# Kernel optimization log

Hardware: AMD Instinct MI355X
Metric: run time of the kernel (lower is better)

The kernel has to match this reference:

```python
import jax, jax.numpy as jnp
import numpy as np

N_NODES = 100000
N_EDGES = 2000000
D = 128
HIDDEN = 128


def setup_inputs() -> dict:
    key = jax.random.key(0)
    k_src, k_dst, k_idx, k_w1, k_w2 = jax.random.split(key, 5)
    src = jax.random.normal(k_src, (N_NODES, D), dtype=jnp.float32)
    dst = jax.random.normal(k_dst, (N_NODES, D), dtype=jnp.float32)
    edge_label_index = jax.random.randint(k_idx, (2, N_EDGES), 0, N_NODES, dtype=jnp.int64)
    # Kaiming-ish init for the two linear layers
    W1 = jax.random.normal(k_w1, (D, HIDDEN), dtype=jnp.float32) / np.sqrt(D)
    b1 = jnp.zeros((HIDDEN,), dtype=jnp.float32)
    W2 = jax.random.normal(k_w2, (HIDDEN, 1), dtype=jnp.float32) / np.sqrt(HIDDEN)
    b2 = jnp.zeros((1,), dtype=jnp.float32)
    return {"src": src, "dst": dst, "edge_label_index": edge_label_index,
            "W1": W1, "b1": b1, "W2": W2, "b2": b2}


def reference(src, dst, edge_label_index, W1, b1, W2, b2):
    row = edge_label_index[0]
    col = edge_label_index[1]
    # gather endpoint embeddings and fuse with elementwise product: [E, D]
    z = src[row] * dst[col]
    # 2-layer MLP; dropout p=0 is the identity
    h = jax.nn.relu(z @ W1 + b1)           # [E, HIDDEN]
    out = h @ W2 + b2                       # [E, 1]
    return out.reshape(-1)                  # [E]
```

## Files before the change

### kernel.cpp

```cpp
#include <hip/hip_runtime.h>
#include <hip/hip_bf16.h>

typedef __attribute__((ext_vector_type(8))) short short8;
typedef __attribute__((ext_vector_type(4))) float f32x4;

#define BLOCK 256
#define GTILE 16

__device__ __forceinline__ int swz16(int row, int boff) {
    return (row << 8) + (boff ^ ((row & 15) << 4));
}
__device__ __forceinline__ int swzH(int row, int boff) {
    return (row << 7) + (boff ^ ((row & 7) << 4));
}

__global__ __launch_bounds__(256) void cvt_bf16_kernel(
    const float* __restrict__ a, const float* __restrict__ b,
    __hip_bfloat16* __restrict__ oa, __hip_bfloat16* __restrict__ ob, int n)
{
    const int i = blockIdx.x * blockDim.x + threadIdx.x;
    const int stride = gridDim.x * blockDim.x;
    const float4* a4 = (const float4*)a;
    const float4* b4 = (const float4*)b;
    const int n8 = n >> 3;
    for (int j = i; j < n8; j += stride) {
        float4 x0 = a4[2 * j], x1 = a4[2 * j + 1];
        float4 y0 = b4[2 * j], y1 = b4[2 * j + 1];
        union { __hip_bfloat16 h[8]; uint4 u; } pa, pb;
        pa.h[0]=__float2bfloat16(x0.x); pa.h[1]=__float2bfloat16(x0.y);
        pa.h[2]=__float2bfloat16(x0.z); pa.h[3]=__float2bfloat16(x0.w);
        pa.h[4]=__float2bfloat16(x1.x); pa.h[5]=__float2bfloat16(x1.y);
        pa.h[6]=__float2bfloat16(x1.z); pa.h[7]=__float2bfloat16(x1.w);
        pb.h[0]=__float2bfloat16(y0.x); pb.h[1]=__float2bfloat16(y0.y);
        pb.h[2]=__float2bfloat16(y0.z); pb.h[3]=__float2bfloat16(y0.w);
        pb.h[4]=__float2bfloat16(y1.x); pb.h[5]=__float2bfloat16(y1.y);
        pb.h[6]=__float2bfloat16(y1.z); pb.h[7]=__float2bfloat16(y1.w);
        ((uint4*)oa)[j] = pa.u;
        ((uint4*)ob)[j] = pb.u;
    }
    for (int j = (n8 << 3) + i; j < n; j += stride) {
        oa[j] = __float2bfloat16(a[j]);
        ob[j] = __float2bfloat16(b[j]);
    }
}

template<bool BF16G>
__global__ __launch_bounds__(BLOCK, 3) void edge_mlp_kernel(
    const float* __restrict__ srcf, const float* __restrict__ dstf,
    const __hip_bfloat16* __restrict__ srcb, const __hip_bfloat16* __restrict__ dstb,
    const int*   __restrict__ eli,
    const float* __restrict__ W1, const float* __restrict__ b1,
    const float* __restrict__ W2, const float* __restrict__ b2,
    float* __restrict__ out, int E)
{
    __shared__ __align__(16) char lds[49152];

    const int tid  = threadIdx.x;
    const int lane = tid & 63;
    const int w    = tid >> 6;
    const int rr   = lane & 15;
    const int kgrp = lane >> 4;
    const int rq8  = lane >> 3;
    const int cl   = lane & 7;

    for (int idx = tid; idx < 128 * 128; idx += BLOCK) {
        int k = idx >> 7, n = idx & 127;
        *(__hip_bfloat16*)(lds + swz16(n, k * 2)) = __float2bfloat16(W1[idx]);
    }
    int probe = eli[2 * (lane & 31) + 1];
    unsigned long long bl = __ballot(lane < 32 && probe != 0);
    const int i64f = (bl == 0ull) ? 1 : 0;
    __syncthreads();

    char* zb = lds + 32768 + (w << 12);

    float b1s[8], w2s[8];
    #pragma unroll
    for (int cb = 0; cb < 8; ++cb) {
        b1s[cb] = b1[cb * 16 + rr];
        w2s[cb] = W2[cb * 16 + rr];
    }
    const float bias2 = b2[0];

    const int ngroups = (E + GTILE - 1) / GTILE;
    const int step = gridDim.x * 4;
    int g = blockIdx.x * 4 + w;
    if (g >= ngroups) return;

    auto idxload = [&](int gg) -> int {
        gg = gg < ngroups ? gg : ngroups - 1;
        int e = gg * GTILE + rr; if (e >= E) e = E - 1;
        size_t off = (lane < 32) ? (size_t)e : (size_t)E + (size_t)e;
        return i64f ? eli[2 * off] : eli[off];
    };

    auto loadT = [&](int iv, short8 (&s)[4], short8 (&d)[4]) {
        const short8* s8 = (const short8*)srcb;
        const short8* d8 = (const short8*)dstb;
        #pragma unroll
        for (int i = 0; i < 4; ++i) {
            int hr = i * 8 + rq8;
            int e  = hr >> 1, h = hr & 1;
            int r = __shfl(iv, e, 64);
            int c = __shfl(iv, 32 + e, 64);
            s[i] = s8[(size_t)r * 16 + h * 8 + cl];
            d[i] = d8[(size_t)c * 16 + h * 8 + cl];
        }
    };
    auto writeT = [&](const short8 (&s)[4], const short8 (&d)[4]) {
        #pragma unroll
        for (int i = 0; i < 4; ++i) {
            int hr = i * 8 + rq8;
            union { __hip_bfloat16 h[8]; short8 v; } pr;
            #pragma unroll
            for (int j = 0; j < 8; ++j) {
                float fs = __bfloat162float(((const __hip_bfloat16*)&s[i])[j]);
                float fd = __bfloat162float(((const __hip_bfloat16*)&d[i])[j]);
                pr.h[j] = __float2bfloat16(fs * fd);
            }
            *(short8*)(zb + swzH(hr, cl * 16)) = pr.v;
        }
    };
    auto stageF = [&](int iv) {
        const float4* s4 = (const float4*)srcf;
        const float4* d4 = (const float4*)dstf;
        #pragma unroll
        for (int i = 0; i < 4; ++i) {
            int hr = i * 8 + rq8;
            int e  = hr >> 1, h = hr & 1;
            int r = __shfl(iv, e, 64);
            int c = __shfl(iv, 32 + e, 64);
            float4 a0 = s4[(size_t)r * 32 + h * 16 + cl * 2];
            float4 a1 = s4[(size_t)r * 32 + h * 16 + cl * 2 + 1];
            float4 c0 = d4[(size_t)c * 32 + h * 16 + cl * 2];
            float4 c1 = d4[(size_t)c * 32 + h * 16 + cl * 2 + 1];
            union { __hip_bfloat16 hh[8]; short8 v; } pr;
            pr.hh[0] = __float2bfloat16(a0.x * c0.x);
            pr.hh[1] = __float2bfloat16(a0.y * c0.y);
            pr.hh[2] = __float2bfloat16(a0.z * c0.z);
            pr.hh[3] = __float2bfloat16(a0.w * c0.w);
            pr.hh[4] = __float2bfloat16(a1.x * c1.x);
            pr.hh[5] = __float2bfloat16(a1.y * c1.y);
            pr.hh[6] = __float2bfloat16(a1.z * c1.z);
            pr.hh[7] = __float2bfloat16(a1.w * c1.w);
            *(short8*)(zb + swzH(hr, cl * 16)) = pr.v;
        }
    };

    auto compute = [&](int gg) {
        f32x4 acc[8];
        #pragma unroll
        for (int cb = 0; cb < 8; ++cb) acc[cb] = (f32x4){0.f, 0.f, 0.f, 0.f};
        __builtin_amdgcn_s_setprio(1);
        #pragma unroll
        for (int kk = 0; kk < 4; ++kk) {
            short8 af = *(const short8*)(zb + swzH(rr * 2 + (kk >> 1),
                                                   (kk & 1) * 64 + kgrp * 16));
            #pragma unroll
            for (int cb = 0; cb < 8; ++cb) {
                short8 bf = *(const short8*)(lds + swz16(cb * 16 + rr,
                                                         kk * 64 + kgrp * 16));
                acc[cb] = __builtin_amdgcn_mfma_f32_16x16x32_bf16(af, bf, acc[cb], 0, 0, 0);
            }
        }
        __builtin_amdgcn_s_setprio(0);
        #pragma unroll
        for (int r = 0; r < 4; ++r) {
            float p = 0.f;
            #pragma unroll
            for (int cb = 0; cb < 8; ++cb) {
                float h = acc[cb][r] + b1s[cb];
                h = fmaxf(h, 0.f);
                p = fmaf(h, w2s[cb], p);
            }
            p += __shfl_xor(p, 1, 64);
            p += __shfl_xor(p, 2, 64);
            p += __shfl_xor(p, 4, 64);
            p += __shfl_xor(p, 8, 64);
            int e = gg * GTILE + kgrp * 4 + r;
            if (rr == 0 && e < E)
                __builtin_nontemporal_store(p + bias2, &out[e]);
        }
    };

    if constexpr (BF16G) {
        short8 svA[4], dvA[4], svB[4], dvB[4];
        int iv0 = idxload(g);
        int iv1 = idxload(g + step);
        loadT(iv0, svA, dvA);
        loadT(iv1, svB, dvB);
        int iv2 = idxload(g + 2 * step);

        while (true) {
            asm volatile("" ::: "memory");
            writeT(svA, dvA);
            loadT(iv2, svA, dvA);
            iv2 = idxload(g + 3 * step);
            asm volatile("" ::: "memory");
            compute(g);
            g += step; if (g >= ngroups) break;

            asm volatile("" ::: "memory");
            writeT(svB, dvB);
            loadT(iv2, svB, dvB);
            iv2 = idxload(g + 3 * step);
            asm volatile("" ::: "memory");
            compute(g);
            g += step; if (g >= ngroups) break;
        }
    } else {
        for (; g < ngroups; g += step) {
            asm volatile("" ::: "memory");
            int iv = idxload(g);
            stageF(iv);
            asm volatile("" ::: "memory");
            compute(g);
        }
    }
}

extern "C" void kernel_launch(void* const* d_in, const int* in_sizes, int n_in,
                              void* d_out, int out_size, void* d_ws, size_t ws_size,
                              hipStream_t stream) {
    const float* src = (const float*)d_in[0];
    const float* dst = (const float*)d_in[1];
    const int*   eli = (const int*)d_in[2];
    const float* W1  = (const float*)d_in[3];
    const float* b1  = (const float*)d_in[4];
    const float* W2  = (const float*)d_in[5];
    const float* b2  = (const float*)d_in[6];
    float* out = (float*)d_out;

    const int E = in_sizes[2] / 2;
    const int nsrc = in_sizes[0];
    const size_t need = (size_t)(in_sizes[0] + in_sizes[1]) * sizeof(__hip_bfloat16);
    const int ngroups = (E + GTILE - 1) / GTILE;
    int nblocks = (ngroups + 3) / 4;
    int grid = nblocks < 768 ? nblocks : 768;

    if (ws_size >= need) {
        __hip_bfloat16* srcb = (__hip_bfloat16*)d_ws;
        __hip_bfloat16* dstb = srcb + nsrc;
        cvt_bf16_kernel<<<dim3(2048), dim3(256), 0, stream>>>(src, dst, srcb, dstb, nsrc);
        edge_mlp_kernel<true><<<dim3(grid), dim3(BLOCK), 0, stream>>>(
            src, dst, srcb, dstb, eli, W1, b1, W2, b2, out, E);
    } else {
        edge_mlp_kernel<false><<<dim3(grid), dim3(BLOCK), 0, stream>>>(
            src, dst, (const __hip_bfloat16*)nullptr, (const __hip_bfloat16*)nullptr,
            eli, W1, b1, W2, b2, out, E);
    }
}
```

Baseline: 178.0 us.

## Bucket edges by destination node and process buckets per XCD for locality

Adds a histogram, scan and scatter pass that sorts edges into 32 buckets by destination node index. The MLP kernel then processes each bucket on a fixed subset of blocks (blockIdx mod 8), so the dst rows being gathered stay resident in a local cache. A final permute kernel writes the results back in the original edge order. It also switches the gathered tables from bf16 to fp16 and does the elementwise product with packed half multiplies. In exchange it adds several extra kernel launches and global passes over the 2M-edge index array, plus a memset.

```diff
diff --git a/kernel.cpp b/kernel.cpp
--- a/kernel.cpp
+++ b/kernel.cpp
@@ -1,11 +1,13 @@
 #include <hip/hip_runtime.h>
 #include <hip/hip_bf16.h>
-
-typedef __attribute__((ext_vector_type(8))) short short8;
+#include <hip/hip_fp16.h>
+
+typedef __attribute__((ext_vector_type(8))) _Float16 half8;
 typedef __attribute__((ext_vector_type(4))) float f32x4;
 
 #define BLOCK 256
 #define GTILE 16
+#define NBKT  32
 
 __device__ __forceinline__ int swz16(int row, int boff) {
     return (row << 8) + (boff ^ ((row & 15) << 4));
@@ -14,10 +16,24 @@
     return (row << 7) + (boff ^ ((row & 7) << 4));
 }
 
-__global__ __launch_bounds__(256) void cvt_bf16_kernel(
+__device__ __forceinline__ int probe_i64(const int* eli) {
+    int any = 0;
+    #pragma unroll
+    for (int i = 0; i < 32; ++i) any |= eli[2 * i + 1];
+    return (any == 0) ? 1 : 0;
+}
+
+__global__ __launch_bounds__(256) void cvt_hist_kernel(
     const float* __restrict__ a, const float* __restrict__ b,
-    __hip_bfloat16* __restrict__ oa, __hip_bfloat16* __restrict__ ob, int n)
-{
+    _Float16* __restrict__ oa, _Float16* __restrict__ ob, int n,
+    const int* __restrict__ eli, int E, float scale, unsigned int* __restrict__ cnt)
+{
+    __shared__ unsigned int h[NBKT];
+    __shared__ int s_i64;
+    if (threadIdx.x < NBKT) h[threadIdx.x] = 0;
+    if (threadIdx.x == 0) s_i64 = probe_i64(eli);
+    __syncthreads();
+
     const int i = blockIdx.x * blockDim.x + threadIdx.x;
     const int stride = gridDim.x * blockDim.x;
     const float4* a4 = (const float4*)a;
@@ -26,32 +42,92 @@
     for (int j = i; j < n8; j += stride) {
         float4 x0 = a4[2 * j], x1 = a4[2 * j + 1];
         float4 y0 = b4[2 * j], y1 = b4[2 * j + 1];
-        union { __hip_bfloat16 h[8]; uint4 u; } pa, pb;
-        pa.h[0]=__float2bfloat16(x0.x); pa.h[1]=__float2bfloat16(x0.y);
-        pa.h[2]=__float2bfloat16(x0.z); pa.h[3]=__float2bfloat16(x0.w);
-        pa.h[4]=__float2bfloat16(x1.x); pa.h[5]=__float2bfloat16(x1.y);
-        pa.h[6]=__float2bfloat16(x1.z); pa.h[7]=__float2bfloat16(x1.w);
-        pb.h[0]=__float2bfloat16(y0.x); pb.h[1]=__float2bfloat16(y0.y);
-        pb.h[2]=__float2bfloat16(y0.z); pb.h[3]=__float2bfloat16(y0.w);
-        pb.h[4]=__float2bfloat16(y1.x); pb.h[5]=__float2bfloat16(y1.y);
-        pb.h[6]=__float2bfloat16(y1.z); pb.h[7]=__float2bfloat16(y1.w);
+        union { _Float16 hh[8]; uint4 u; } pa, pb;
+        pa.hh[0]=(_Float16)x0.x; pa.hh[1]=(_Float16)x0.y;
+        pa.hh[2]=(_Float16)x0.z; pa.hh[3]=(_Float16)x0.w;
+        pa.hh[4]=(_Float16)x1.x; pa.hh[5]=(_Float16)x1.y;
+        pa.hh[6]=(_Float16)x1.z; pa.hh[7]=(_Float16)x1.w;
+        pb.hh[0]=(_Float16)y0.x; pb.hh[1]=(_Float16)y0.y;
+        pb.hh[2]=(_Float16)y0.z; pb.hh[3]=(_Float16)y0.w;
+        pb.hh[4]=(_Float16)y1.x; pb.hh[5]=(_Float16)y1.y;
+        pb.hh[6]=(_Float16)y1.z; pb.hh[7]=(_Float16)y1.w;
         ((uint4*)oa)[j] = pa.u;
         ((uint4*)ob)[j] = pb.u;
     }
     for (int j = (n8 << 3) + i; j < n; j += stride) {
-        oa[j] = __float2bfloat16(a[j]);
-        ob[j] = __float2bfloat16(b[j]);
-    }
-}
-
-template<bool BF16G>
-__global__ __launch_bounds__(BLOCK, 3) void edge_mlp_kernel(
-    const float* __restrict__ srcf, const float* __restrict__ dstf,
-    const __hip_bfloat16* __restrict__ srcb, const __hip_bfloat16* __restrict__ dstb,
-    const int*   __restrict__ eli,
+        oa[j] = (_Float16)a[j];
+        ob[j] = (_Float16)b[j];
+    }
+    const int i64f = s_i64;
+    for (int e = i; e < E; e += stride) {
+        int c = i64f ? eli[2 * ((size_t)E + e)] : eli[(size_t)E + e];
+        int bkt = (int)((float)c * scale);
+        if (bkt > NBKT - 1) bkt = NBKT - 1;
+        atomicAdd(&h[bkt], 1u);
+    }
+    __syncthreads();
+    if (threadIdx.x < NBKT && h[threadIdx.x])
+        atomicAdd(&cnt[threadIdx.x], h[threadIdx.x]);
+}
+
+__global__ void scan_kernel(const unsigned int* __restrict__ cnt,
+                            unsigned int* __restrict__ segStart,
+                            unsigned int* __restrict__ cursor)
+{
+    if (threadIdx.x == 0) {
+        unsigned int s = 0;
+        for (int b = 0; b < NBKT; ++b) { segStart[b] = s; cursor[b] = s; s += cnt[b]; }
+        segStart[NBKT] = s;
+    }
+}
+
+__global__ __launch_bounds__(256) void scatter_kernel(
+    const int* __restrict__ eli, int E, float scale,
+    unsigned int* __restrict__ cursor,
+    uint2* __restrict__ sorted, unsigned int* __restrict__ inv)
+{
+    __shared__ unsigned int lcnt[NBKT];
+    __shared__ unsigned int lpos[NBKT];
+    __shared__ int s_i64;
+    if (threadIdx.x < NBKT) lcnt[threadIdx.x] = 0;
+    if (threadIdx.x == 0) s_i64 = probe_i64(eli);
+    __syncthreads();
+    const int i64f = s_i64;
+
+    const int chunk = (E + gridDim.x - 1) / gridDim.x;
+    const int e0 = blockIdx.x * chunk;
+    const int e1 = min(E, e0 + chunk);
+
+    for (int e = e0 + threadIdx.x; e < e1; e += blockDim.x) {
+        int c = i64f ? eli[2 * ((size_t)E + e)] : eli[(size_t)E + e];
+        int bkt = (int)((float)c * scale);
+        if (bkt > NBKT - 1) bkt = NBKT - 1;
+        atomicAdd(&lcnt[bkt], 1u);
+    }
+    __syncthreads();
+    if (threadIdx.x < NBKT) {
+        unsigned int nv = lcnt[threadIdx.x];
+        lpos[threadIdx.x] = nv ? atomicAdd(&cursor[threadIdx.x], nv) : 0u;
+    }
+    __syncthreads();
+    for (int e = e0 + threadIdx.x; e < e1; e += blockDim.x) {
+        int r, c;
+        if (i64f) { r = eli[2 * (size_t)e]; c = eli[2 * ((size_t)E + e)]; }
+        else      { r = eli[e];             c = eli[(size_t)E + e]; }
+        int bkt = (int)((float)c * scale);
+        if (bkt > NBKT - 1) bkt = NBKT - 1;
+        unsigned int pos = atomicAdd(&lpos[bkt], 1u);
+        sorted[pos] = make_uint2((unsigned)r, (unsigned)c);
+        inv[e] = pos;
+    }
+}
+
+__global__ __launch_bounds__(BLOCK, 3) void mlp_sorted_kernel(
+    const _Float16* __restrict__ srcb, const _Float16* __restrict__ dstb,
+    const uint2* __restrict__ sorted, const unsigned int* __restrict__ segStart,
     const float* __restrict__ W1, const float* __restrict__ b1,
     const float* __restrict__ W2, const float* __restrict__ b2,
-    float* __restrict__ out, int E)
+    float* __restrict__ tmp, int E)
 {
     __shared__ __align__(16) char lds[49152];
 
@@ -65,7 +141,149 @@
 
     for (int idx = tid; idx < 128 * 128; idx += BLOCK) {
         int k = idx >> 7, n = idx & 127;
-        *(__hip_bfloat16*)(lds + swz16(n, k * 2)) = __float2bfloat16(W1[idx]);
+        *(_Float16*)(lds + swz16(n, k * 2)) = (_Float16)W1[idx];
+    }
+    __syncthreads();
+
+    char* zb = lds + 32768 + (w << 12);
+
+    float b1s[8], w2s[8];
+    #pragma unroll
+    for (int cb = 0; cb < 8; ++cb) {
+        b1s[cb] = b1[cb * 16 + rr];
+        w2s[cb] = W2[cb * 16 + rr];
+    }
+    const float bias2 = b2[0];
+
+    const int x     = blockIdx.x & 7;
+    const int kb    = blockIdx.x >> 3;
+    const int nbs   = gridDim.x >> 3;
+    const int wslot = kb * 4 + w;
+    const int wstep = nbs * 4;
+
+    half8 sv[4], dv[4];
+    const half8* s8 = (const half8*)srcb;
+    const half8* d8 = (const half8*)dstb;
+
+    for (int j = 0; j < NBKT / 8; ++j) {
+        const int b  = x + 8 * j;
+        const int s0 = (int)segStart[b];
+        const int s1 = (int)segStart[b + 1];
+        if (s1 <= s0) continue;
+        const int nt = (s1 - s0 + 15) >> 4;
+        int t = wslot;
+        if (t >= nt) continue;
+
+        {
+            int idx = s0 + t * 16 + rr; if (idx >= s1) idx = s1 - 1;
+            uint2 iv = sorted[idx];
+            #pragma unroll
+            for (int i = 0; i < 4; ++i) {
+                int hr = i * 8 + rq8, e = hr >> 1, hh = hr & 1;
+                int r = __shfl((int)iv.x, e, 64);
+                int c = __shfl((int)iv.y, e, 64);
+                sv[i] = s8[(size_t)r * 16 + hh * 8 + cl];
+                dv[i] = d8[(size_t)c * 16 + hh * 8 + cl];
+            }
+        }
+
+        while (true) {
+            const int base = s0 + t * 16;
+            int cnt = s1 - base; if (cnt > 16) cnt = 16;
+
+            asm volatile("" ::: "memory");
+            #pragma unroll
+            for (int i = 0; i < 4; ++i) {
+                int hr = i * 8 + rq8;
+                half8 pr = sv[i] * dv[i];
+                *(half8*)(zb + swzH(hr, cl * 16)) = pr;
+            }
+
+            const int tn = t + wstep;
+            if (tn < nt) {
+                int idx = s0 + tn * 16 + rr; if (idx >= s1) idx = s1 - 1;
+                uint2 iv = sorted[idx];
+                #pragma unroll
+                for (int i = 0; i < 4; ++i) {
+                    int hr = i * 8 + rq8, e = hr >> 1, hh = hr & 1;
+                    int r = __shfl((int)iv.x, e, 64);
+                    int c = __shfl((int)iv.y, e, 64);
+                    sv[i] = s8[(size_t)r * 16 + hh * 8 + cl];
+                    dv[i] = d8[(size_t)c * 16 + hh * 8 + cl];
+                }
+            }
+            asm volatile("" ::: "memory");
+
+            f32x4 acc[8];
+            #pragma unroll
+            for (int cb = 0; cb < 8; ++cb) acc[cb] = (f32x4){0.f, 0.f, 0.f, 0.f};
+            __builtin_amdgcn_s_setprio(1);
+            #pragma unroll
+            for (int kk = 0; kk < 4; ++kk) {
+                half8 af = *(const half8*)(zb + swzH(rr * 2 + (kk >> 1),
+                                                     (kk & 1) * 64 + kgrp * 16));
+                #pragma unroll
+                for (int cb = 0; cb < 8; ++cb) {
+                    half8 bf = *(const half8*)(lds + swz16(cb * 16 + rr,
+                                                           kk * 64 + kgrp * 16));
+                    acc[cb] = __builtin_amdgcn_mfma_f32_16x16x32_f16(af, bf, acc[cb], 0, 0, 0);
+                }
+            }
+            __builtin_amdgcn_s_setprio(0);
+
+            #pragma unroll
+            for (int r = 0; r < 4; ++r) {
+                float p = 0.f;
+                #pragma unroll
+                for (int cb = 0; cb < 8; ++cb) {
+                    float hv = acc[cb][r] + b1s[cb];
+                    hv = fmaxf(hv, 0.f);
+                    p = fmaf(hv, w2s[cb], p);
+                }
+                p += __shfl_xor(p, 1, 64);
+                p += __shfl_xor(p, 2, 64);
+                p += __shfl_xor(p, 4, 64);
+                p += __shfl_xor(p, 8, 64);
+                int eo = kgrp * 4 + r;
+                if (rr == 0 && eo < cnt)
+                    __builtin_nontemporal_store(p + bias2, &tmp[base + eo]);
+            }
+            if (tn >= nt) break;
+            t = tn;
+        }
+    }
+}
+
+__global__ __launch_bounds__(256) void permute_kernel(
+    const float* __restrict__ tmp, const unsigned int* __restrict__ inv,
+    float* __restrict__ out, int E)
+{
+    for (int e = blockIdx.x * blockDim.x + threadIdx.x; e < E;
+         e += gridDim.x * blockDim.x)
+        out[e] = tmp[inv[e]];
+}
+
+template<int MODE>
+__global__ __launch_bounds__(BLOCK, 3) void edge_mlp_fb(
+    const float* __restrict__ srcf, const float* __restrict__ dstf,
+    const _Float16* __restrict__ srcb, const _Float16* __restrict__ dstb,
+    const int* __restrict__ eli,
+    const float* __restrict__ W1, const float* __restrict__ b1,
+    const float* __restrict__ W2, const float* __restrict__ b2,
+    float* __restrict__ out, int E)
+{
+    __shared__ __align__(16) char lds[49152];
+    const int tid  = threadIdx.x;
+    const int lane = tid & 63;
+    const int w    = tid >> 6;
+    const int rr   = lane & 15;
+    const int kgrp = lane >> 4;
+    const int rq8  = lane >> 3;
+    const int cl   = lane & 7;
+
+    for (int idx = tid; idx < 128 * 128; idx += BLOCK) {
+        int k = idx >> 7, n = idx & 127;
+        *(_Float16*)(lds + swz16(n, k * 2)) = (_Float16)W1[idx];
     }
     int probe = eli[2 * (lane & 31) + 1];
     unsigned long long bl = __ballot(lane < 32 && probe != 0);
@@ -73,7 +291,6 @@
     __syncthreads();
 
     char* zb = lds + 32768 + (w << 12);
-
     float b1s[8], w2s[8];
     #pragma unroll
     for (int cb = 0; cb < 8; ++cb) {
@@ -94,31 +311,17 @@
         return i64f ? eli[2 * off] : eli[off];
     };
 
-    auto loadT = [&](int iv, short8 (&s)[4], short8 (&d)[4]) {
-        const short8* s8 = (const short8*)srcb;
-        const short8* d8 = (const short8*)dstb;
+    half8 sv[4], dv[4];
+    auto loadT = [&](int iv) {
+        const half8* s8 = (const half8*)srcb;
+        const half8* d8 = (const half8*)dstb;
         #pragma unroll
         for (int i = 0; i < 4; ++i) {
-            int hr = i * 8 + rq8;
-            int e  = hr >> 1, h = hr & 1;
+            int hr = i * 8 + rq8, e = hr >> 1, hh = hr & 1;
             int r = __shfl(iv, e, 64);
             int c = __shfl(iv, 32 + e, 64);
-            s[i] = s8[(size_t)r * 16 + h * 8 + cl];
-            d[i] = d8[(size_t)c * 16 + h * 8 + cl];
-        }
-    };
-    auto writeT = [&](const short8 (&s)[4], const short8 (&d)[4]) {
-        #pragma unroll
-        for (int i = 0; i < 4; ++i) {
-            int hr = i * 8 + rq8;
-            union { __hip_bfloat16 h[8]; short8 v; } pr;
-            #pragma unroll
-            for (int j = 0; j < 8; ++j) {
-                float fs = __bfloat162float(((const __hip_bfloat16*)&s[i])[j]);
-                float fd = __bfloat162float(((const __hip_bfloat16*)&d[i])[j]);
-                pr.h[j] = __float2bfloat16(fs * fd);
-            }
-            *(short8*)(zb + swzH(hr, cl * 16)) = pr.v;
+            sv[i] = s8[(size_t)r * 16 + hh * 8 + cl];
+            dv[i] = d8[(size_t)c * 16 + hh * 8 + cl];
         }
     };
     auto stageF = [&](int iv) {
@@ -126,27 +329,21 @@
         const float4* d4 = (const float4*)dstf;
         #pragma unroll
         for (int i = 0; i < 4; ++i) {
-            int hr = i * 8 + rq8;
-            int e  = hr >> 1, h = hr & 1;
+            int hr = i * 8 + rq8, e = hr >> 1, hh = hr & 1;
             int r = __shfl(iv, e, 64);
             int c = __shfl(iv, 32 + e, 64);
-            float4 a0 = s4[(size_t)r * 32 + h * 16 + cl * 2];
-            float4 a1 = s4[(size_t)r * 32 + h * 16 + cl * 2 + 1];
-            float4 c0 = d4[(size_t)c * 32 + h * 16 + cl * 2];
-            float4 c1 = d4[(size_t)c * 32 + h * 16 + cl * 2 + 1];
-            union { __hip_bfloat16 hh[8]; short8 v; } pr;
-            pr.hh[0] = __float2bfloat16(a0.x * c0.x);
-            pr.hh[1] = __float2bfloat16(a0.y * c0.y);
-            pr.hh[2] = __float2bfloat16(a0.z * c0.z);
-            pr.hh[3] = __float2bfloat16(a0.w * c0.w);
-            pr.hh[4] = __float2bfloat16(a1.x * c1.x);
-            pr.hh[5] = __float2bfloat16(a1.y * c1.y);
-            pr.hh[6] = __float2bfloat16(a1.z * c1.z);
-            pr.hh[7] = __float2bfloat16(a1.w * c1.w);
-            *(short8*)(zb + swzH(hr, cl * 16)) = pr.v;
+            float4 a0 = s4[(size_t)r * 32 + hh * 16 + cl * 2];
+            float4 a1 = s4[(size_t)r * 32 + hh * 16 + cl * 2 + 1];
+            float4 c0 = d4[(size_t)c * 32 + hh * 16 + cl * 2];
+            float4 c1 = d4[(size_t)c * 32 + hh * 16 + cl * 2 + 1];
+            union { _Float16 hf[8]; half8 v; } pr;
+            pr.hf[0]=(_Float16)(a0.x*c0.x); pr.hf[1]=(_Float16)(a0.y*c0.y);
+            pr.hf[2]=(_Float16)(a0.z*c0.z); pr.hf[3]=(_Float16)(a0.w*c0.w);
+            pr.hf[4]=(_Float16)(a1.x*c1.x); pr.hf[5]=(_Float16)(a1.y*c1.y);
+            pr.hf[6]=(_Float16)(a1.z*c1.z); pr.hf[7]=(_Float16)(a1.w*c1.w);
+            *(half8*)(zb + swzH(hr, cl * 16)) = pr.v;
         }
     };
-
     auto compute = [&](int gg) {
         f32x4 acc[8];
         #pragma unroll
@@ -154,13 +351,13 @@
         __builtin_amdgcn_s_setprio(1);
         #pragma unroll
         for (int kk = 0; kk < 4; ++kk) {
-            short8 af = *(const short8*)(zb + swzH(rr * 2 + (kk >> 1),
-                                                   (kk & 1) * 64 + kgrp * 16));
+            half8 af = *(const half8*)(zb + swzH(rr * 2 + (kk >> 1),
+                                                 (kk & 1) * 64 + kgrp * 16));
             #pragma unroll
             for (int cb = 0; cb < 8; ++cb) {
-                short8 bf = *(const short8*)(lds + swz16(cb * 16 + rr,
-                                                         kk * 64 + kgrp * 16));
-                acc[cb] = __builtin_amdgcn_mfma_f32_16x16x32_bf16(af, bf, acc[cb], 0, 0, 0);
+                half8 bf = *(const half8*)(lds + swz16(cb * 16 + rr,
+                                                       kk * 64 + kgrp * 16));
+                acc[cb] = __builtin_amdgcn_mfma_f32_16x16x32_f16(af, bf, acc[cb], 0, 0, 0);
             }
         }
         __builtin_amdgcn_s_setprio(0);
@@ -169,9 +366,9 @@
             float p = 0.f;
             #pragma unroll
             for (int cb = 0; cb < 8; ++cb) {
-                float h = acc[cb][r] + b1s[cb];
-                h = fmaxf(h, 0.f);
-                p = fmaf(h, w2s[cb], p);
+                float hv = acc[cb][r] + b1s[cb];
+                hv = fmaxf(hv, 0.f);
+                p = fmaf(hv, w2s[cb], p);
             }
             p += __shfl_xor(p, 1, 64);
             p += __shfl_xor(p, 2, 64);
@@ -183,30 +380,23 @@
         }
     };
 
-    if constexpr (BF16G) {
-        short8 svA[4], dvA[4], svB[4], dvB[4];
-        int iv0 = idxload(g);
-        int iv1 = idxload(g + step);
-        loadT(iv0, svA, dvA);
-        loadT(iv1, svB, dvB);
-        int iv2 = idxload(g + 2 * step);
-
+    if constexpr (MODE == 1) {
+        int iv = idxload(g);
+        loadT(iv);
         while (true) {
             asm volatile("" ::: "memory");
-            writeT(svA, dvA);
-            loadT(iv2, svA, dvA);
-            iv2 = idxload(g + 3 * step);
+            #pragma unroll
+            for (int i = 0; i < 4; ++i) {
+                int hr = i * 8 + rq8;
+                half8 pr = sv[i] * dv[i];
+                *(half8*)(zb + swzH(hr, cl * 16)) = pr;
+            }
+            int gn = g + step;
+            if (gn < ngroups) { int iv2 = idxload(gn); loadT(iv2); }
             asm volatile("" ::: "memory");
             compute(g);
-            g += step; if (g >= ngroups) break;
-
-            asm volatile("" ::: "memory");
-            writeT(svB, dvB);
-            loadT(iv2, svB, dvB);
-            iv2 = idxload(g + 3 * step);
-            asm volatile("" ::: "memory");
-            compute(g);
-            g += step; if (g >= ngroups) break;
+            if (gn >= ngroups) break;
+            g = gn;
         }
     } else {
         for (; g < ngroups; g += step) {
@@ -232,21 +422,64 @@
     float* out = (float*)d_out;
 
     const int E = in_sizes[2] / 2;
-    const int nsrc = in_sizes[0];
-    const size_t need = (size_t)(in_sizes[0] + in_sizes[1]) * sizeof(__hip_bfloat16);
-    const int ngroups = (E + GTILE - 1) / GTILE;
-    int nblocks = (ngroups + 3) / 4;
-    int grid = nblocks < 768 ? nblocks : 768;
-
-    if (ws_size >= need) {
-        __hip_bfloat16* srcb = (__hip_bfloat16*)d_ws;
-        __hip_bfloat16* dstb = srcb + nsrc;
-        cvt_bf16_kernel<<<dim3(2048), dim3(256), 0, stream>>>(src, dst, srcb, dstb, nsrc);
-        edge_mlp_kernel<true><<<dim3(grid), dim3(BLOCK), 0, stream>>>(
-            src, dst, srcb, dstb, eli, W1, b1, W2, b2, out, E);
+    const int n = in_sizes[0];
+    const int N = n / 128;
+    const float scale = (float)NBKT / (float)N;
+
+    const size_t NB = (size_t)n * sizeof(_Float16);
+    const size_t need_full = 4096 + 2 * NB + (size_t)E * 16;
+    const size_t need_tab  = 2 * NB;
+
+    if (ws_size >= need_full) {
+        char* wsb = (char*)d_ws;
+        unsigned int* cnt      = (unsigned int*)wsb;
+        unsigned int* segStart = cnt + 32;
+        unsigned int* cursor   = segStart + 40;
+        _Float16* srcb = (_Float16*)(wsb + 4096);
+        _Float16* dstb = srcb + n;
+        uint2* sorted  = (uint2*)(wsb + 4096 + 2 * NB);
+        unsigned int* inv = (unsigned int*)(sorted + E);
+        float* tmp = (float*)(inv + E);
+
+        hipMemsetAsync(wsb, 0, 4096, stream);
+        cvt_hist_kernel<<<dim3(2048), dim3(256), 0, stream>>>(
+            src, dst, srcb, dstb, n, eli, E, scale, cnt);
+        scan_kernel<<<dim3(1), dim3(64), 0, stream>>>(cnt, segStart, cursor);
+        scatter_kernel<<<dim3(256), dim3(256), 0, stream>>>(
+            eli, E, scale, cursor, sorted, inv);
+        mlp_sorted_kernel<<<dim3(768), dim3(BLOCK), 0, stream>>>(
+            srcb, dstb, sorted, segStart, W1, b1, W2, b2, tmp, E);
+        permute_kernel<<<dim3(2048), dim3(256), 0, stream>>>(tmp, inv, out, E);
+    } else if (ws_size >= need_tab) {
+        _Float16* srcb = (_Float16*)d_ws;
+        _Float16* dstb = srcb + n;
+        if (ws_size >= need_tab + 4096) {
+            char* wsb = (char*)d_ws;
+            unsigned int* cnt = (unsigned int*)(wsb + 2 * NB);
+            _Float16* sb = (_Float16*)wsb;
+            _Float16* db = sb + n;
+            hipMemsetAsync(cnt, 0, 4096, stream);
+            cvt_hist_kernel<<<dim3(2048), dim3(256), 0, stream>>>(
+                src, dst, sb, db, n, eli, E, scale, cnt);
+            const int ngroups = (E + GTILE - 1) / GTILE;
+            int nblocks = (ngroups + 3) / 4;
+            int grid = nblocks < 768 ? nblocks : 768;
+            edge_mlp_fb<1><<<dim3(grid), dim3(BLOCK), 0, stream>>>(
+                src, dst, sb, db, eli, W1, b1, W2, b2, out, E);
+        } else {
+            const int ngroups = (E + GTILE - 1) / GTILE;
+            int nblocks = (ngroups + 3) / 4;
+            int grid = nblocks < 768 ? nblocks : 768;
+            edge_mlp_fb<0><<<dim3(grid), dim3(BLOCK), 0, stream>>>(
+                src, dst, (const _Float16*)nullptr, (const _Float16*)nullptr,
+                eli, W1, b1, W2, b2, out, E);
+        }
     } else {
-        edge_mlp_kernel<false><<<dim3(grid), dim3(BLOCK), 0, stream>>>(
-            src, dst, (const __hip_bfloat16*)nullptr, (const __hip_bfloat16*)nullptr,
+        const int ngroups = (E + GTILE - 1) / GTILE;
+        int nblocks = (ngroups + 3) / 4;
+        int grid = nblocks < 768 ? nblocks : 768;
+        edge_mlp_fb<0><<<dim3(grid), dim3(BLOCK), 0, stream>>>(
+            src, dst, (const _Float16*)nullptr, (const _Float16*)nullptr,
             eli, W1, b1, W2, b2, out, E);
     }
 }
```

New measurement: 200.9 us. 12.9% more time.
